# Optimization experiments

Measured on AMD Instinct MI355X. Metric: run time of the kernel, lower is better.

The kernel has to match this reference:

```python
import jax, jax.numpy as jnp
import numpy as np
from jax import lax

DIM = 1024
D_STATE = 64
D_CONV = 4
EXPAND = 2
HEADDIM = 64
D_INNER = EXPAND * DIM            # 2048
NHEADS = D_INNER // HEADDIM       # 32
NGROUPS = 1
CONV_DIM = D_INNER + 2 * NGROUPS * D_STATE      # 2176
D_IN_PROJ = 2 * D_INNER + 2 * NGROUPS * D_STATE + NHEADS  # 4256
BATCH, SEQLEN = 2, 4096
EPS = 1e-5


def setup_inputs() -> dict:
    key = jax.random.key(0)
    ks = jax.random.split(key, 10)
    X = jax.random.normal(ks[0], (BATCH, SEQLEN, DIM), dtype=jnp.float32)
    in_proj_w = jax.random.normal(ks[1], (D_IN_PROJ, DIM), dtype=jnp.float32) * 0.02
    conv_w = jax.random.normal(ks[2], (CONV_DIM, 1, D_CONV), dtype=jnp.float32) * 0.2
    conv_b = jax.random.normal(ks[3], (CONV_DIM,), dtype=jnp.float32) * 0.02
    dt_bias = jax.random.normal(ks[4], (NHEADS,), dtype=jnp.float32) * 0.5 - 2.0
    A_log = jnp.log(jax.random.uniform(ks[5], (NHEADS,), minval=1.0, maxval=16.0))
    D = jax.random.normal(ks[6], (NHEADS,), dtype=jnp.float32)
    norm_w = jnp.ones((D_INNER,), dtype=jnp.float32)
    out_proj_w = jax.random.normal(ks[7], (DIM, D_INNER), dtype=jnp.float32) * 0.02
    to_h_w = jax.random.normal(ks[8], (2 * DIM, DIM), dtype=jnp.float32) * 0.02
    return dict(X=X, in_proj_w=in_proj_w, conv_w=conv_w, conv_b=conv_b,
                dt_bias=dt_bias, A_log=A_log, D=D, norm_w=norm_w,
                out_proj_w=out_proj_w, to_h_w=to_h_w)


def _silu(x):
    return x * jax.nn.sigmoid(x)


def _mamba2(X, in_proj_w, conv_w, conv_b, dt_bias, A_log, D, norm_w, out_proj_w):
    Bsz, L, _ = X.shape
    zxbcdt = jnp.einsum('bld,ed->ble', X, in_proj_w)  # (B,L,D_IN_PROJ)
    z = zxbcdt[..., :D_INNER]
    xBC = zxbcdt[..., D_INNER:D_INNER + CONV_DIM]
    dt_raw = zxbcdt[..., D_INNER + CONV_DIM:]
    dt = jax.nn.softplus(dt_raw + dt_bias)  # (B,L,H)

    # causal depthwise conv over time, then silu
    xc = jnp.transpose(xBC, (0, 2, 1))                       # (B,C,L)
    xc = jnp.pad(xc, ((0, 0), (0, 0), (D_CONV - 1, 0)))
    xc = lax.conv_general_dilated(xc, conv_w, window_strides=(1,), padding='VALID',
                                  dimension_numbers=('NCH', 'OIH', 'NCH'),
                                  feature_group_count=CONV_DIM)
    xc = xc + conv_b[None, :, None]
    xBC = _silu(jnp.transpose(xc, (0, 2, 1)))                # (B,L,C)

    x = xBC[..., :D_INNER].reshape(Bsz, L, NHEADS, HEADDIM)  # (B,L,H,P)
    Bm = xBC[..., D_INNER:D_INNER + D_STATE]                 # (B,L,N) ngroups=1
    Cm = xBC[..., D_INNER + D_STATE:]                        # (B,L,N)

    A = -jnp.exp(A_log)                                      # (H,)

    def step(h, inp):
        dt_t, B_t, C_t, x_t = inp   # (B,H), (B,N), (B,N), (B,H,P)
        dA = jnp.exp(dt_t * A)                               # (B,H)
        h = h * dA[..., None, None] + jnp.einsum('bh,bhp,bn->bhpn', dt_t, x_t, B_t)
        y_t = jnp.einsum('bhpn,bn->bhp', h, C_t)
        return h, y_t

    h0 = jnp.zeros((Bsz, NHEADS, HEADDIM, D_STATE), dtype=X.dtype)
    xs = (jnp.moveaxis(dt, 1, 0), jnp.moveaxis(Bm, 1, 0),
          jnp.moveaxis(Cm, 1, 0), jnp.moveaxis(x, 1, 0))
    _, ys = lax.scan(step, h0, xs)                           # (L,B,H,P)
    y = jnp.moveaxis(ys, 0, 1) + x * D[None, None, :, None]  # skip term
    y = y.reshape(Bsz, L, D_INNER)

    # gated RMSNorm: rmsnorm(y * silu(z)) * weight
    y = y * _silu(z)
    y = y * lax.rsqrt(jnp.mean(y * y, axis=-1, keepdims=True) + EPS) * norm_w
    return jnp.einsum('bld,ed->ble', y, out_proj_w)          # (B,L,DIM)


def reference(X, in_proj_w, conv_w, conv_b, dt_bias, A_log, D, norm_w, out_proj_w, to_h_w):
    H = _mamba2(X, in_proj_w, conv_w, conv_b, dt_bias, A_log, D, norm_w, out_proj_w)
    HKV = jnp.einsum('bld,ed->ble', H, to_h_w)               # (B,L,2*DIM)
    HK, HV = HKV[..., :DIM], HKV[..., DIM:]
    return (HK, HV)
```

## Files before the change

kernel.cpp:

```cpp
#include <hip/hip_runtime.h>
#include <hip/hip_bf16.h>
#include <math.h>

#define B_       2
#define L_       4096
#define DIM_     1024
#define DINNER_  2048
#define DSTATE_  64
#define NH_      32
#define HD_      64
#define CONVDIM_ 2176
#define DIP_     4256
#define M_       (B_*L_)
#define XRW_     2208
#define NC_      64

typedef __attribute__((ext_vector_type(8))) short short8;
typedef __attribute__((ext_vector_type(4))) float floatx4;
typedef __hip_bfloat16 bf16;

__device__ __forceinline__ float bf2f(unsigned short u) {
    unsigned int v = ((unsigned int)u) << 16;
    return __builtin_bit_cast(float, v);
}
__device__ __forceinline__ unsigned short f2bf(float f) {
    unsigned int x = __builtin_bit_cast(unsigned int, f);
    unsigned int lsb = (x >> 16) & 1u;
    x += 0x7fffu + lsb;
    return (unsigned short)(x >> 16);
}
__device__ __forceinline__ void storeo(bf16* p, float v) {
    *reinterpret_cast<unsigned short*>(p) = f2bf(v);
}
__device__ __forceinline__ void storeo(float* p, float v) { *p = v; }

__device__ __forceinline__ void gl2lds16(const bf16* g, short* lds) {
    __builtin_amdgcn_global_load_lds(
        (const __attribute__((address_space(1))) void*)g,
        (__attribute__((address_space(3))) void*)lds, 16, 0, 0);
}

__global__ __launch_bounds__(256) void cast2_k(
    const float* __restrict__ s1, bf16* __restrict__ d1,
    const float* __restrict__ s2, bf16* __restrict__ d2, int nb1)
{
    const float* src;
    bf16* dst;
    size_t i0;
    if ((int)blockIdx.x < nb1) {
        src = s1; dst = d1;
        i0 = ((size_t)blockIdx.x * 256 + threadIdx.x) * 8;
    } else {
        src = s2; dst = d2;
        i0 = ((size_t)(blockIdx.x - nb1) * 256 + threadIdx.x) * 8;
    }
    uint4 a = *reinterpret_cast<const uint4*>(src + i0);
    uint4 b = *reinterpret_cast<const uint4*>(src + i0 + 4);
    unsigned int w0 = (unsigned int)f2bf(__builtin_bit_cast(float, a.x)) |
                      ((unsigned int)f2bf(__builtin_bit_cast(float, a.y)) << 16);
    unsigned int w1 = (unsigned int)f2bf(__builtin_bit_cast(float, a.z)) |
                      ((unsigned int)f2bf(__builtin_bit_cast(float, a.w)) << 16);
    unsigned int w2 = (unsigned int)f2bf(__builtin_bit_cast(float, b.x)) |
                      ((unsigned int)f2bf(__builtin_bit_cast(float, b.y)) << 16);
    unsigned int w3 = (unsigned int)f2bf(__builtin_bit_cast(float, b.z)) |
                      ((unsigned int)f2bf(__builtin_bit_cast(float, b.w)) << 16);
    *reinterpret_cast<uint4*>(reinterpret_cast<unsigned short*>(dst) + i0) =
        make_uint4(w0, w1, w2, w3);
}

__global__ __launch_bounds__(256) void wprep_k(
    const float* __restrict__ Wop, bf16* __restrict__ WopT,
    const float* __restrict__ Wth, bf16* __restrict__ Wthb)
{
    __shared__ unsigned short t[64][72];
    if (blockIdx.x < 512) {
        const int R = 1024, C = 2048;
        int nct = C >> 6;
        int r0 = ((int)blockIdx.x / nct) << 6;
        int c0 = ((int)blockIdx.x % nct) << 6;
        int tr = threadIdx.x >> 2;
        int tc = (threadIdx.x & 3) << 4;
        const float* s = Wop + (size_t)(r0 + tr) * C + c0 + tc;
#pragma unroll
        for (int k = 0; k < 16; k += 4) {
            float4 v = *reinterpret_cast<const float4*>(s + k);
            t[tr][tc + k + 0] = f2bf(v.x);
            t[tr][tc + k + 1] = f2bf(v.y);
            t[tr][tc + k + 2] = f2bf(v.z);
            t[tr][tc + k + 3] = f2bf(v.w);
        }
        __syncthreads();
        unsigned short* d = (unsigned short*)WopT + (size_t)(c0 + tr) * R + r0 + tc;
        unsigned int ww[8];
#pragma unroll
        for (int q = 0; q < 8; q++)
            ww[q] = (unsigned int)t[tc + 2*q][tr] | ((unsigned int)t[tc + 2*q + 1][tr] << 16);
        *reinterpret_cast<uint4*>(d)     = make_uint4(ww[0], ww[1], ww[2], ww[3]);
        *reinterpret_cast<uint4*>(d + 8) = make_uint4(ww[4], ww[5], ww[6], ww[7]);
    } else {
        size_t i0 = ((size_t)(blockIdx.x - 512) * 256 + threadIdx.x) * 8;
        uint4 a = *reinterpret_cast<const uint4*>(Wth + i0);
        uint4 b = *reinterpret_cast<const uint4*>(Wth + i0 + 4);
        unsigned int w0 = (unsigned int)f2bf(__builtin_bit_cast(float, a.x)) |
                          ((unsigned int)f2bf(__builtin_bit_cast(float, a.y)) << 16);
        unsigned int w1 = (unsigned int)f2bf(__builtin_bit_cast(float, a.z)) |
                          ((unsigned int)f2bf(__builtin_bit_cast(float, a.w)) << 16);
        unsigned int w2 = (unsigned int)f2bf(__builtin_bit_cast(float, b.x)) |
                          ((unsigned int)f2bf(__builtin_bit_cast(float, b.y)) << 16);
        unsigned int w3 = (unsigned int)f2bf(__builtin_bit_cast(float, b.z)) |
                          ((unsigned int)f2bf(__builtin_bit_cast(float, b.w)) << 16);
        *reinterpret_cast<uint4*>(reinterpret_cast<unsigned short*>(Wthb) + i0) =
            make_uint4(w0, w1, w2, w3);
    }
}

template <typename TO>
__global__ __launch_bounds__(256) void gemm_bt16(
    const bf16* __restrict__ A, const bf16* __restrict__ W,
    TO* __restrict__ outA, TO* __restrict__ outB,
    int M, int N, int K, int split, int strideA, int strideB)
{
    __shared__ short As[128*64];
    __shared__ short Ws[128*64];
    const int tid  = threadIdx.x;
    const int m0   = blockIdx.y * 128;
    const int n0   = blockIdx.x * 128;
    const int wave = tid >> 6;
    const int lane = tid & 63;
    const int wm   = (wave >> 1) * 64;
    const int wn   = (wave & 1) * 64;
    const int ln   = lane & 15;
    const int quad = lane >> 4;
    const int lr   = lane >> 3;
    const int lc   = (lane & 7) * 8;

    floatx4 acc[4][4];
#pragma unroll
    for (int i = 0; i < 4; i++)
#pragma unroll
        for (int j = 0; j < 4; j++) acc[i][j] = (floatx4){0.f, 0.f, 0.f, 0.f};

    for (int k0 = 0; k0 < K; k0 += 64) {
#pragma unroll
        for (int it = 0; it < 4; it++) {
            int ig = wave * 4 + it;
            gl2lds16(A + (size_t)(m0 + ig * 8 + lr) * K + k0 + lc, &As[ig * 512]);
            gl2lds16(W + (size_t)(n0 + ig * 8 + lr) * K + k0 + lc, &Ws[ig * 512]);
        }
        __syncthreads();
#pragma unroll
        for (int kk = 0; kk < 64; kk += 32) {
            short8 af[4], bfv[4];
#pragma unroll
            for (int i = 0; i < 4; i++)
                af[i] = *reinterpret_cast<const short8*>(&As[(wm + i * 16 + ln) * 64 + kk + quad * 8]);
#pragma unroll
            for (int j = 0; j < 4; j++)
                bfv[j] = *reinterpret_cast<const short8*>(&Ws[(wn + j * 16 + ln) * 64 + kk + quad * 8]);
#pragma unroll
            for (int i = 0; i < 4; i++)
#pragma unroll
                for (int j = 0; j < 4; j++)
                    acc[i][j] = __builtin_amdgcn_mfma_f32_16x16x32_bf16(af[i], bfv[j], acc[i][j], 0, 0, 0);
        }
        __syncthreads();
    }

#pragma unroll
    for (int i = 0; i < 4; i++)
#pragma unroll
        for (int j = 0; j < 4; j++)
#pragma unroll
            for (int r = 0; r < 4; r++) {
                int grow = m0 + wm + i * 16 + quad * 4 + r;
                int gcol = n0 + wn + j * 16 + ln;
                if (gcol < N) {
                    if (gcol < split)
                        storeo(outA + (size_t)grow * strideA + gcol, acc[i][j][r]);
                    else
                        storeo(outB + (size_t)grow * strideB + (gcol - split), acc[i][j][r]);
                }
            }
}

template <typename TO>
__global__ __launch_bounds__(512, 2) void gemm256(
    const bf16* __restrict__ Ag, const bf16* __restrict__ Wg,
    TO* __restrict__ outA, TO* __restrict__ outB,
    int M, int N, int K, int split, int strideA, int strideB, int nbx)
{
    __shared__ short lds[65536];

    const int tid  = threadIdx.x;
    const int wave = tid >> 6;
    const int lane = tid & 63;
    const int ln   = lane & 15;
    const int quad = lane >> 4;
    const int wr   = wave >> 2;
    const int wc   = wave & 3;
    const int bh   = wc >> 1;
    const int wcl  = wc & 1;
    const int xorv = (ln & 7) << 4;

    int nwg  = gridDim.x;
    int orig = blockIdx.x;
    int wg   = ((nwg & 7) == 0) ? ((orig & 7) * (nwg >> 3) + (orig >> 3)) : orig;
    const int bx = wg % nbx;
    const int by = wg / nbx;
    const int m0 = by * 256;
    const int n0 = bx * 256;

    int lo0 = tid * 16;
    int lo1 = 8192 + tid * 16;
    int so0 = lo0 ^ (((lo0 >> 7) & 7) << 4);
    int so1 = lo1 ^ (((lo1 >> 7) & 7) << 4);
    const int srow0 = so0 >> 7, scol0 = (so0 & 127) >> 1;
    const int srow1 = so1 >> 7, scol1 = (so1 & 127) >> 1;

#define STG_A(bufb, h, kc) do {                                               \
    short* dst_ = &lds[((bufb)*2 + (h)) * 8192 + wave * 512];                 \
    gl2lds16(Ag + (size_t)(m0 + (h)*128 + srow0) * K + (kc) + scol0, dst_);   \
    gl2lds16(Ag + (size_t)(m0 + (h)*128 + srow1) * K + (kc) + scol1, dst_ + 4096); \
} while (0)
#define STG_B(bufb, h, kc) do {                                               \
    short* dst_ = &lds[32768 + ((bufb)*2 + (h)) * 8192 + wave * 512];         \
    gl2lds16(Wg + (size_t)(n0 + (h)*128 + srow0) * K + (kc) + scol0, dst_);   \
    gl2lds16(Wg + (size_t)(n0 + (h)*128 + srow1) * K + (kc) + scol1, dst_ + 4096); \
} while (0)

#define RD_A(qi) do {                                                         \
    const char* Ab_ = (const char*)&lds[(cur*2 + wr) * 8192];                 \
    _Pragma("unroll") for (int i = 0; i < 4; i++)                             \
    _Pragma("unroll") for (int ks = 0; ks < 2; ks++)                          \
        af[i][ks] = *reinterpret_cast<const short8*>(                         \
            Ab_ + ((((qi)*64 + i*16 + ln)*128 + ks*64 + quad*16) ^ xorv));    \
} while (0)
#define RD_B(qj, BV) do {                                                     \
    const char* Bb_ = (const char*)&lds[32768 + (cur*2 + bh) * 8192];         \
    _Pragma("unroll") for (int j = 0; j < 2; j++)                             \
    _Pragma("unroll") for (int ks = 0; ks < 2; ks++)                          \
        BV[j][ks] = *reinterpret_cast<const short8*>(                         \
            Bb_ + (((wcl*64 + (qj)*32 + j*16 + ln)*128 + ks*64 + quad*16) ^ xorv)); \
} while (0)

#define MMA(qi, qj, BV) do {                                                  \
    _Pragma("unroll") for (int i = 0; i < 4; i++)                             \
    _Pragma("unroll") for (int j = 0; j < 2; j++)                             \
    _Pragma("unroll") for (int ks = 0; ks < 2; ks++)                          \
        acc[(qi)*4+i][(qj)*2+j] = __builtin_amdgcn_mfma_f32_16x16x32_bf16(    \
            af[i][ks], BV[j][ks], acc[(qi)*4+i][(qj)*2+j], 0, 0, 0);          \
} while (0)

    floatx4 acc[8][4];
#pragma unroll
    for (int i = 0; i < 8; i++)
#pragma unroll
        for (int j = 0; j < 4; j++) acc[i][j] = (floatx4){0.f, 0.f, 0.f, 0.f};

    const int NT = K >> 6;

    STG_A(0, 0, 0); STG_A(0, 1, 0);
    STG_B(0, 0, 0); STG_B(0, 1, 0);
    asm volatile("s_waitcnt vmcnt(0)" ::: "memory");
    __builtin_amdgcn_s_barrier();
    __builtin_amdgcn_sched_barrier(0);

    short8 af[4][2], bf0[2][2], bf1[2][2];

    for (int t = 0; t < NT; ++t) {
        const int cur = t & 1, nxt = cur ^ 1;
        const int kc  = (t + 1) << 6;
        const bool pf = (t + 1 < NT);

        RD_A(0);
        RD_B(0, bf0);
        RD_B(1, bf1);

        if (pf) {
            STG_A(nxt, 0, kc); STG_A(nxt, 1, kc);
            STG_B(nxt, 0, kc); STG_B(nxt, 1, kc);
        }

        __builtin_amdgcn_s_setprio(1);
        MMA(0, 0, bf0);
        MMA(0, 1, bf1);
        RD_A(1);
        MMA(1, 1, bf1);
        MMA(1, 0, bf0);
        __builtin_amdgcn_s_setprio(0);

        if (pf) { asm volatile("s_waitcnt vmcnt(0)" ::: "memory"); }
        __builtin_amdgcn_s_barrier();
        __builtin_amdgcn_sched_barrier(0);
    }

#undef STG_A
#undef STG_B
#undef RD_A
#undef RD_B
#undef MMA

#pragma unroll
    for (int qi = 0; qi < 2; qi++)
#pragma unroll
    for (int i = 0; i < 4; i++)
#pragma unroll
    for (int qj = 0; qj < 2; qj++)
#pragma unroll
    for (int j = 0; j < 2; j++)
#pragma unroll
    for (int r = 0; r < 4; r++) {
        int grow = m0 + wr*128 + qi*64 + i*16 + quad*4 + r;
        int gcol = n0 + wc*64 + qj*32 + j*16 + ln;
        float v = acc[qi*4+i][qj*2+j][r];
        if (gcol < N) {
            if (gcol < split)
                storeo(outA + (size_t)grow * strideA + gcol, v);
            else
                storeo(outB + (size_t)grow * strideB + (gcol - split), v);
        }
    }
}

__global__ __launch_bounds__(256) void conv_dt_k(
    const bf16* __restrict__ xr, const float* __restrict__ cw,
    const float* __restrict__ cb, const float* __restrict__ dtb,
    bf16* __restrict__ xc, float* __restrict__ dtf)
{
    int idx = blockIdx.x * 256 + threadIdx.x;
    int row = idx / 276;
    int g   = idx - row * 276;
    const unsigned short* xru = (const unsigned short*)xr;

    if (g >= 272) {
        int h0 = (g - 272) * 8;
        uint4 rv = *reinterpret_cast<const uint4*>(xru + (size_t)row * XRW_ + 2176 + h0);
        const unsigned int* w = &rv.x;
        float o[8];
#pragma unroll
        for (int k = 0; k < 8; k++) {
            unsigned short u = (k & 1) ? (unsigned short)(w[k >> 1] >> 16)
                                       : (unsigned short)(w[k >> 1] & 0xffffu);
            float v = bf2f(u) + dtb[h0 + k];
            o[k] = fmaxf(v, 0.f) + log1pf(__expf(-fabsf(v)));
        }
        *reinterpret_cast<float4*>(&dtf[(size_t)row * NH_ + h0]) =
            make_float4(o[0], o[1], o[2], o[3]);
        *reinterpret_cast<float4*>(&dtf[(size_t)row * NH_ + h0 + 4]) =
            make_float4(o[4], o[5], o[6], o[7]);
        return;
    }

    int ch0 = g * 8;
    int t   = row & (L_ - 1);
    uint4 rv[4];
#pragma unroll
    for (int j = 0; j < 4; j++) {
        rv[j] = make_uint4(0u, 0u, 0u, 0u);
        if (t + j - 3 >= 0)
            rv[j] = *reinterpret_cast<const uint4*>(xru + (size_t)(row + j - 3) * XRW_ + ch0);
    }
    unsigned int ow[4];
#pragma unroll
    for (int pair = 0; pair < 4; pair++) {
        unsigned short o2[2];
#pragma unroll
        for (int k = 0; k < 2; k++) {
            int cc = pair * 2 + k;
            float a = cb[ch0 + cc];
#pragma unroll
            for (int j = 0; j < 4; j++) {
                unsigned int w32 = (&rv[j].x)[cc >> 1];
                unsigned short u = (cc & 1) ? (unsigned short)(w32 >> 16)
                                            : (unsigned short)(w32 & 0xffffu);
                a = fmaf(bf2f(u), cw[(ch0 + cc) * 4 + j], a);
            }
            o2[k] = f2bf(a / (1.f + __expf(-a)));
        }
        ow[pair] = (unsigned int)o2[0] | ((unsigned int)o2[1] << 16);
    }
    *reinterpret_cast<uint4*>((unsigned short*)xc + (size_t)row * CONVDIM_ + ch0) =
        make_uint4(ow[0], ow[1], ow[2], ow[3]);
}

__global__ __launch_bounds__(256) void chunk_intra_k(
    const bf16* __restrict__ xc, const float* __restrict__ dtf,
    const float* __restrict__ A_log, const float* __restrict__ Dp,
    bf16* __restrict__ Yg, float* __restrict__ Sg, float* __restrict__ Eg)
{
    __shared__ short Bst[64*72];
    __shared__ short Cst[64*72];
    __shared__ short xsM[64*72];
    __shared__ short xT [64*72];
    __shared__ short BwT[64*72];
    __shared__ float dts[64], cums[64], wS[64];

    const int tid  = threadIdx.x;
    const int bid  = blockIdx.x;
    const int h    = bid & 31;
    const int bc   = bid >> 5;
    const int c    = bc & 63;
    const int b    = bc >> 6;
    const int xch0 = h * 64;
    const unsigned short* xcu = (const unsigned short*)xc;

    const float Ah = -__expf(A_log[h]);
    const float Dh = Dp[h];

    for (int q = tid; q < 1536; q += 256) {
        int sel = q >> 9;
        int qq  = q & 511;
        int r = qq >> 3, c8 = (qq & 7) * 8;
        size_t ro = (size_t)(b * L_ + c * 64 + r) * CONVDIM_;
        if (sel == 0)
            *reinterpret_cast<uint4*>(&Bst[r*72 + c8]) =
                *reinterpret_cast<const uint4*>(xcu + ro + 2048 + c8);
        else if (sel == 1)
            *reinterpret_cast<uint4*>(&Cst[r*72 + c8]) =
                *reinterpret_cast<const uint4*>(xcu + ro + 2112 + c8);
        else
            *reinterpret_cast<uint4*>(&xsM[r*72 + c8]) =
                *reinterpret_cast<const uint4*>(xcu + ro + xch0 + c8);
    }
    if (tid < 64) dts[tid] = dtf[(size_t)(b * L_ + c * 64 + tid) * NH_ + h];
    __syncthreads();

    if (tid < 64) {
        float v = dts[tid] * Ah;
#pragma unroll
        for (int o = 1; o < 64; o <<= 1) {
            float u = __shfl_up(v, o, 64);
            if (tid >= o) v += u;
        }
        cums[tid] = v;
    }
    __syncthreads();
    if (tid < 64) wS[tid] = __expf(cums[63] - cums[tid]) * dts[tid];
    if (tid == 0) Eg[bid] = __expf(cums[63]);
    __syncthreads();

    for (int q = tid; q < 4096; q += 256) {
        int s = q & 63, ch = q >> 6;
        xT [ch*72 + s] = xsM[s*72 + ch];
        BwT[ch*72 + s] = (short)f2bf(bf2f((unsigned short)Bst[s*72 + ch]) * wS[s]);
    }
    __syncthreads();

    const int wave = tid >> 6, lane = tid & 63;
    const int ln = lane & 15, quad = lane >> 4;
    const int wm = (wave >> 1) * 32, wn = (wave & 1) * 32;

    floatx4 accG[2][2];
#pragma unroll
    for (int i = 0; i < 2; i++)
#pragma unroll
        for (int j = 0; j < 2; j++) accG[i][j] = (floatx4){0.f,0.f,0.f,0.f};
#pragma unroll
    for (int kk = 0; kk < 64; kk += 32) {
        short8 af[2], bfv[2];
#pragma unroll
        for (int i = 0; i < 2; i++)
            af[i] = *reinterpret_cast<const short8*>(&Cst[(wm + i*16 + ln)*72 + kk + quad*8]);
#pragma unroll
        for (int j = 0; j < 2; j++)
            bfv[j] = *reinterpret_cast<const short8*>(&Bst[(wn + j*16 + ln)*72 + kk + quad*8]);
#pragma unroll
        for (int i = 0; i < 2; i++)
#pragma unroll
            for (int j = 0; j < 2; j++)
                accG[i][j] = __builtin_amdgcn_mfma_f32_16x16x32_bf16(af[i], bfv[j], accG[i][j], 0,0,0);
    }
    __syncthreads();
#pragma unroll
    for (int i = 0; i < 2; i++)
#pragma unroll
        for (int j = 0; j < 2; j++)
#pragma unroll
            for (int r = 0; r < 4; r++) {
                int t = wm + i*16 + quad*4 + r;
                int s = wn + j*16 + ln;
                float v = (s <= t) ? __expf(cums[t] - cums[s]) * dts[s] * accG[i][j][r] : 0.f;
                xsM[t*72 + s] = (short)f2bf(v);
            }
    __syncthreads();

    floatx4 accY[2][2];
#pragma unroll
    for (int i = 0; i < 2; i++)
#pragma unroll
        for (int j = 0; j < 2; j++) accY[i][j] = (floatx4){0.f,0.f,0.f,0.f};
#pragma unroll
    for (int kk = 0; kk < 64; kk += 32) {
        short8 af[2], bfv[2];
#pragma unroll
        for (int i = 0; i < 2; i++)
            af[i] = *reinterpret_cast<const short8*>(&xsM[(wm + i*16 + ln)*72 + kk + quad*8]);
#pragma unroll
        for (int j = 0; j < 2; j++)
            bfv[j] = *reinterpret_cast<const short8*>(&xT[(wn + j*16 + ln)*72 + kk + quad*8]);
#pragma unroll
        for (int i = 0; i < 2; i++)
#pragma unroll
            for (int j = 0; j < 2; j++)
                accY[i][j] = __builtin_amdgcn_mfma_f32_16x16x32_bf16(af[i], bfv[j], accY[i][j], 0,0,0);
    }
    unsigned short* Yu = (unsigned short*)Yg;
#pragma unroll
    for (int i = 0; i < 2; i++)
#pragma unroll
        for (int j = 0; j < 2; j++)
#pragma unroll
            for (int r = 0; r < 4; r++) {
                int t = wm + i*16 + quad*4 + r;
                int p = wn + j*16 + ln;
                float yv = accY[i][j][r] + Dh * bf2f((unsigned short)xT[p*72 + t]);
                Yu[(size_t)(b*L_ + c*64 + t)*DINNER_ + xch0 + p] = f2bf(yv);
            }

    floatx4 accS[2][2];
#pragma unroll
    for (int i = 0; i < 2; i++)
#pragma unroll
        for (int j = 0; j < 2; j++) accS[i][j] = (floatx4){0.f,0.f,0.f,0.f};
#pragma unroll
    for (int kk = 0; kk < 64; kk += 32) {
        short8 af[2], bfv[2];
#pragma unroll
        for (int i = 0; i < 2; i++)
            af[i] = *reinterpret_cast<const short8*>(&xT[(wm + i*16 + ln)*72 + kk + quad*8]);
#pragma unroll
        for (int j = 0; j < 2; j++)
            bfv[j] = *reinterpret_cast<const short8*>(&BwT[(wn + j*16 + ln)*72 + kk + quad*8]);
#pragma unroll
        for (int i = 0; i < 2; i++)
#pragma unroll
            for (int j = 0; j < 2; j++)
                accS[i][j] = __builtin_amdgcn_mfma_f32_16x16x32_bf16(af[i], bfv[j], accS[i][j], 0,0,0);
    }
#pragma unroll
    for (int i = 0; i < 2; i++)
#pragma unroll
        for (int j = 0; j < 2; j++)
#pragma unroll
            for (int r = 0; r < 4; r++) {
                int p = wm + i*16 + quad*4 + r;
                int n = wn + j*16 + ln;
                Sg[(size_t)bid * 4096 + p*64 + n] = accS[i][j][r];
            }
}

__global__ __launch_bounds__(256) void chunk_state_k(
    float* __restrict__ Sg, const float* __restrict__ Eg)
{
    int g  = blockIdx.x * 1024 + threadIdx.x * 4;
    int bh = g >> 12;
    int b  = bh >> 5, h = bh & 31;
    int e  = g & 4095;
    float4 run = make_float4(0.f, 0.f, 0.f, 0.f);
    for (int c = 0; c < NC_; c++) {
        int bid = (b * 64 + c) * 32 + h;
        size_t idx = (size_t)bid * 4096 + e;
        float4 s = *reinterpret_cast<float4*>(&Sg[idx]);
        float  E = Eg[bid];
        *reinterpret_cast<float4*>(&Sg[idx]) = run;
        run.x = run.x * E + s.x;
        run.y = run.y * E + s.y;
        run.z = run.z * E + s.z;
        run.w = run.w * E + s.w;
    }
}

__global__ __launch_bounds__(256) void chunk_inter_k(
    const bf16* __restrict__ xc, const float* __restrict__ Sg,
    const float* __restrict__ dtf, const float* __restrict__ A_log,
    bf16* __restrict__ Yg)
{
    __shared__ short Cst[64*72];
    __shared__ short hpT[64*72];
    __shared__ float dts[64], wcumL[64];

    const int tid = threadIdx.x;
    const int bid = blockIdx.x;
    const int h   = bid & 31;
    const int bc  = bid >> 5;
    const int c   = bc & 63;
    const int b   = bc >> 6;
    const unsigned short* xcu = (const unsigned short*)xc;

    const float Ah = -__expf(A_log[h]);

    for (int q = tid; q < 512; q += 256) {
        int r = q >> 3, c8 = (q & 7) * 8;
        *reinterpret_cast<uint4*>(&Cst[r*72 + c8]) =
            *reinterpret_cast<const uint4*>(xcu + (size_t)(b*L_ + c*64 + r)*CONVDIM_ + 2112 + c8);
    }
    for (int q = tid; q < 1024; q += 256) {
        int p = q >> 4, n4 = (q & 15) * 4;
        float4 v = *reinterpret_cast<const float4*>(&Sg[(size_t)bid * 4096 + p*64 + n4]);
        unsigned int lo = (unsigned int)f2bf(v.x) | ((unsigned int)f2bf(v.y) << 16);
        unsigned int hi = (unsigned int)f2bf(v.z) | ((unsigned int)f2bf(v.w) << 16);
        *reinterpret_cast<uint2*>(&hpT[p*72 + n4]) = make_uint2(lo, hi);
    }
    if (tid < 64) dts[tid] = dtf[(size_t)(b*L_ + c*64 + tid) * NH_ + h];
    __syncthreads();
    if (tid < 64) {
        float v = dts[tid] * Ah;
#pragma unroll
        for (int o = 1; o < 64; o <<= 1) {
            float u = __shfl_up(v, o, 64);
            if (tid >= o) v += u;
        }
        wcumL[tid] = __expf(v);
    }
    __syncthreads();

    const int wave = tid >> 6, lane = tid & 63;
    const int ln = lane & 15, quad = lane >> 4;
    const int wm = (wave >> 1) * 32, wn = (wave & 1) * 32;

    floatx4 acc[2][2];
#pragma unroll
    for (int i = 0; i < 2; i++)
#pragma unroll
        for (int j = 0; j < 2; j++) acc[i][j] = (floatx4){0.f,0.f,0.f,0.f};
#pragma unroll
    for (int kk = 0; kk < 64; kk += 32) {
        short8 af[2], bfv[2];
#pragma unroll
        for (int i = 0; i < 2; i++)
            af[i] = *reinterpret_cast<const short8*>(&Cst[(wm + i*16 + ln)*72 + kk + quad*8]);
#pragma unroll
        for (int j = 0; j < 2; j++)
            bfv[j] = *reinterpret_cast<const short8*>(&hpT[(wn + j*16 + ln)*72 + kk + quad*8]);
#pragma unroll
        for (int i = 0; i < 2; i++)
#pragma unroll
            for (int j = 0; j < 2; j++)
                acc[i][j] = __builtin_amdgcn_mfma_f32_16x16x32_bf16(af[i], bfv[j], acc[i][j], 0,0,0);
    }
    unsigned short* Yu = (unsigned short*)Yg;
#pragma unroll
    for (int i = 0; i < 2; i++)
#pragma unroll
        for (int j = 0; j < 2; j++)
#pragma unroll
            for (int r = 0; r < 4; r++) {
                int t = wm + i*16 + quad*4 + r;
                int p = wn + j*16 + ln;
                size_t idx = (size_t)(b*L_ + c*64 + t)*DINNER_ + h*64 + p;
                float yv = bf2f(Yu[idx]) + wcumL[t] * acc[i][j][r];
                Yu[idx] = f2bf(yv);
            }
}

__global__ __launch_bounds__(256) void gate_norm_k(
    bf16* __restrict__ y, const bf16* __restrict__ zbuf, const float* __restrict__ nw)
{
    __shared__ float red[4];
    int row = blockIdx.x;
    int tid = threadIdx.x;
    unsigned short* yy = (unsigned short*)y;
    const unsigned short* zz = (const unsigned short*)zbuf;

    uint4 yv = *reinterpret_cast<uint4*>(&yy[(size_t)row * DINNER_ + tid * 8]);
    uint4 zv = *reinterpret_cast<const uint4*>(&zz[(size_t)row * DINNER_ + tid * 8]);
    unsigned int yw[4] = {yv.x, yv.y, yv.z, yv.w};
    unsigned int zw[4] = {zv.x, zv.y, zv.z, zv.w};
    float g[8];
    float ss = 0.f;
#pragma unroll
    for (int q = 0; q < 4; q++) {
        float y0 = bf2f((unsigned short)(yw[q] & 0xffffu)), y1 = bf2f((unsigned short)(yw[q] >> 16));
        float z0 = bf2f((unsigned short)(zw[q] & 0xffffu)), z1 = bf2f((unsigned short)(zw[q] >> 16));
        float g0 = y0 * (z0 / (1.f + __expf(-z0)));
        float g1 = y1 * (z1 / (1.f + __expf(-z1)));
        g[q * 2] = g0; g[q * 2 + 1] = g1;
        ss += g0 * g0 + g1 * g1;
    }
#pragma unroll
    for (int o = 1; o < 64; o <<= 1) ss += __shfl_xor(ss, o);
    if ((tid & 63) == 0) red[tid >> 6] = ss;
    __syncthreads();
    float tot = red[0] + red[1] + red[2] + red[3];
    float rinv = rsqrtf(tot * (1.f / DINNER_) + 1e-5f);

    unsigned int ow[4];
#pragma unroll
    for (int q = 0; q < 4; q++) {
        float w0 = nw[tid * 8 + q * 2];
        float w1 = nw[tid * 8 + q * 2 + 1];
        unsigned short o0 = f2bf(g[q * 2] * rinv * w0);
        unsigned short o1 = f2bf(g[q * 2 + 1] * rinv * w1);
        ow[q] = (unsigned int)o0 | ((unsigned int)o1 << 16);
    }
    *reinterpret_cast<uint4*>(&yy[(size_t)row * DINNER_ + tid * 8]) =
        make_uint4(ow[0], ow[1], ow[2], ow[3]);
}


extern "C" void kernel_launch(void* const* d_in, const int* in_sizes, int n_in,
                              void* d_out, int out_size, void* d_ws, size_t ws_size,
                              hipStream_t stream)
{
    const float* X    = (const float*)d_in[0];
    const float* Wip  = (const float*)d_in[1];
    const float* cw   = (const float*)d_in[2];
    const float* cb   = (const float*)d_in[3];
    const float* dtb  = (const float*)d_in[4];
    const float* Alog = (const float*)d_in[5];
    const float* Dp   = (const float*)d_in[6];
    const float* nw   = (const float*)d_in[7];
    const float* Wop  = (const float*)d_in[8];
    const float* Wth  = (const float*)d_in[9];
    float* out = (float*)d_out;

    char* ws = (char*)d_ws;
    bf16*  zbuf = (bf16*) (ws);
    bf16*  WopT = (bf16*) (ws);
    bf16*  Wthb = (bf16*) (ws + 4194304);
    bf16*  Wc   = (bf16*) (ws + 8388608);
    bf16*  xr   = (bf16*) (ws + 33554432);
    bf16*  Yg   = (bf16*) (ws + 33554432);
    bf16*  xc   = (bf16*) (ws + 69730304);
    bf16*  Xb   = (bf16*) (ws + 69730304);
    bf16*  Wipb = (bf16*) (ws + 69730304 + 16777216);
    float* dtf  = (float*)(ws + 105381888);
    float* Eg   = (float*)(ws + 106430464);
    float* Sg   = (float*)d_out;

    dim3 blk(256);
    dim3 blk512(512);

    cast2_k<<<4096 + 2128, blk, 0, stream>>>(X, Xb, Wip, Wipb, 4096);

    gemm256<bf16><<<dim3(17 * 32), blk512, 0, stream>>>(
        Xb, Wipb, zbuf, xr, M_, DIP_, DIM_, DINNER_, DINNER_, XRW_, 17);

    conv_dt_k<<<(M_ * 276) / 256, blk, 0, stream>>>(xr, cw, cb, dtb, xc, dtf);

    chunk_intra_k<<<B_ * NC_ * NH_, blk, 0, stream>>>(
        xc, dtf, Alog, Dp, Yg, Sg, Eg);
    chunk_state_k<<<256, blk, 0, stream>>>(Sg, Eg);
    chunk_inter_k<<<B_ * NC_ * NH_, blk, 0, stream>>>(xc, Sg, dtf, Alog, Yg);

    gate_norm_k<<<M_, blk, 0, stream>>>(Yg, zbuf, nw);

    wprep_k<<<512 + 1024, blk, 0, stream>>>(Wop, WopT, Wth, Wthb);
    gemm_bt16<bf16><<<dim3(16, 16), blk, 0, stream>>>(
        Wthb, WopT, Wc, Wc, DINNER_, DINNER_, DIM_, DINNER_, DINNER_, DINNER_);

    gemm256<float><<<dim3(8 * 32), blk512, 0, stream>>>(
        Yg, Wc, out, out + (size_t)M_ * DIM_, M_, DINNER_, DINNER_, DIM_, DIM_, DIM_, 8);
}
```

Measured before the change: 468.1 us.

## Interleave global-to-LDS staging with MFMA phases in GEMM main loop

Restructures the GEMM K-loop into four phases, each issuing one staging load, LDS reads and an MFMA block separated by barriers. B tiles are now prefetched two iterations ahead and A tiles one ahead, with partial vmcnt waits in place of full drains. The aim is to spread global memory traffic across the compute phases and keep more loads in flight. In exchange it adds many more s_barrier calls per iteration, which may cost synchronisation overhead.

```diff
diff --git a/kernel.cpp b/kernel.cpp
--- a/kernel.cpp
+++ b/kernel.cpp
@@ -244,11 +244,13 @@
 } while (0)
 
 #define MMA(qi, qj, BV) do {                                                  \
+    __builtin_amdgcn_s_setprio(1);                                            \
     _Pragma("unroll") for (int i = 0; i < 4; i++)                             \
     _Pragma("unroll") for (int j = 0; j < 2; j++)                             \
     _Pragma("unroll") for (int ks = 0; ks < 2; ks++)                          \
         acc[(qi)*4+i][(qj)*2+j] = __builtin_amdgcn_mfma_f32_16x16x32_bf16(    \
             af[i][ks], BV[j][ks], acc[(qi)*4+i][(qj)*2+j], 0, 0, 0);          \
+    __builtin_amdgcn_s_setprio(0);                                            \
 } while (0)
 
     floatx4 acc[8][4];
@@ -261,35 +263,48 @@
 
     STG_A(0, 0, 0); STG_A(0, 1, 0);
     STG_B(0, 0, 0); STG_B(0, 1, 0);
-    asm volatile("s_waitcnt vmcnt(0)" ::: "memory");
+    if (NT > 1) {
+        STG_B(1, 0, 64); STG_B(1, 1, 64);
+        asm volatile("s_waitcnt vmcnt(4)" ::: "memory");
+    } else {
+        asm volatile("s_waitcnt vmcnt(0)" ::: "memory");
+    }
     __builtin_amdgcn_s_barrier();
     __builtin_amdgcn_sched_barrier(0);
 
     short8 af[4][2], bf0[2][2], bf1[2][2];
 
     for (int t = 0; t < NT; ++t) {
-        const int cur = t & 1, nxt = cur ^ 1;
-        const int kc  = (t + 1) << 6;
-        const bool pf = (t + 1 < NT);
-
-        RD_A(0);
-        RD_B(0, bf0);
+        const int cur = t & 1, oth = cur ^ 1;
+        const int kc1 = (t + 1) << 6;
+        const int kc2 = (t + 2) << 6;
+
+        if (t + 1 < NT) STG_A(oth, 0, kc1);
+        RD_A(0); RD_B(0, bf0);
+        __builtin_amdgcn_s_barrier();
+        MMA(0, 0, bf0);
+        __builtin_amdgcn_s_barrier();
+
+        if (t + 1 < NT) STG_A(oth, 1, kc1);
         RD_B(1, bf1);
-
-        if (pf) {
-            STG_A(nxt, 0, kc); STG_A(nxt, 1, kc);
-            STG_B(nxt, 0, kc); STG_B(nxt, 1, kc);
-        }
-
-        __builtin_amdgcn_s_setprio(1);
-        MMA(0, 0, bf0);
+        __builtin_amdgcn_s_barrier();
         MMA(0, 1, bf1);
+        __builtin_amdgcn_s_barrier();
+
+        if (t + 2 < NT) STG_B(cur, 0, kc2);
         RD_A(1);
+        __builtin_amdgcn_s_barrier();
         MMA(1, 1, bf1);
+        __builtin_amdgcn_s_barrier();
+
+        if (t + 2 < NT) {
+            STG_B(cur, 1, kc2);
+            asm volatile("s_waitcnt vmcnt(4)" ::: "memory");
+        } else if (t + 1 < NT) {
+            asm volatile("s_waitcnt vmcnt(0)" ::: "memory");
+        }
+        __builtin_amdgcn_s_barrier();
         MMA(1, 0, bf0);
-        __builtin_amdgcn_s_setprio(0);
-
-        if (pf) { asm volatile("s_waitcnt vmcnt(0)" ::: "memory"); }
         __builtin_amdgcn_s_barrier();
         __builtin_amdgcn_sched_barrier(0);
     }
```

After: 470.8 us. Within noise of the previous version (+0.6%).
